# Optimization experiments

Measured on AMD Instinct MI355X. Metric: run time of the kernel, lower is better.

Reference implementation:

```python
import jax, jax.numpy as jnp
import numpy as np

K = 8
EPS = 1e-8


def setup_inputs() -> dict:
    key = jax.random.key(0)
    tokens = jax.random.normal(key, (32, 1024, 256), dtype=jnp.float32)
    return {"tokens": tokens}


def reference(tokens) -> jnp.ndarray:
    # tokens: [B, N, D] -> adjacency [B, N, N] float32 (0/1), mutual kNN, no self-loops
    B, N, D = tokens.shape
    tn = tokens / (jnp.linalg.norm(tokens, axis=-1, keepdims=True) + EPS)
    sim = jnp.einsum('bnd,bmd->bnm', tn, tn)  # [B, N, N] cosine similarity
    # mask diagonal (add_self=False)
    diag = jnp.eye(N, dtype=bool)
    sim = jnp.where(diag[None, :, :], -jnp.inf, sim)
    k = min(K, N - 1)
    _, topk_idx = jax.lax.top_k(sim, k)  # [B, N, k]
    b_idx = jnp.arange(B)[:, None, None]
    r_idx = jnp.arange(N)[None, :, None]
    adj = jnp.zeros((B, N, N), dtype=bool).at[b_idx, r_idx, topk_idx].set(True)
    # mutual kNN: keep edge only if both directions selected
    adj = adj & jnp.swapaxes(adj, 1, 2)
    return adj.astype(jnp.float32)
```

## Files before the change

kernel.cpp:

```cpp
#include <hip/hip_runtime.h>
#include <math.h>
#include <stdint.h>

#define B_ 32
#define N_ 1024
#define D_ 256
#define K_ 8
#define CAND 12

typedef unsigned short u16;
typedef unsigned int u32;
typedef __attribute__((ext_vector_type(8))) short s16x8;
typedef __attribute__((ext_vector_type(16))) float f32x16;

__device__ inline void cp16(const void* g, void* l) {
    __builtin_amdgcn_global_load_lds((const __attribute__((address_space(1))) void*)g,
                                     (__attribute__((address_space(3))) void*)l, 16, 0, 0);
}

__device__ inline u16 f2bf(float f) {
    uint32_t u = __float_as_uint(f);
    return (u16)((u + 0x7fffu + ((u >> 16) & 1u)) >> 16);
}
__device__ inline float bf2f(u16 h) { return __uint_as_float(((uint32_t)h) << 16); }
__device__ inline u32 umax32(u32 a, u32 b) { return a > b ? a : b; }
__device__ inline u32 umin32(u32 a, u32 b) { return a < b ? a : b; }

__global__ __launch_bounds__(256) void prep_kernel(const float* __restrict__ tok,
                                                   double* __restrict__ invn,
                                                   u16* __restrict__ xhi,
                                                   u16* __restrict__ xlo) {
    const int tid = threadIdx.x;
    const int wave = tid >> 6, lane = tid & 63;
    const int row = blockIdx.x * 4 + wave;
    const float4 v = *reinterpret_cast<const float4*>(tok + (size_t)row * D_ + lane * 4);
    double s = (double)v.x * v.x + (double)v.y * v.y +
               (double)v.z * v.z + (double)v.w * v.w;
    #pragma unroll
    for (int off = 32; off > 0; off >>= 1) s += __shfl_xor(s, off, 64);
    const double inv = 1.0 / (sqrt(s) + 1e-8);
    if (lane == 0) invn[row] = inv;
    const float x0 = (float)(v.x * inv), x1 = (float)(v.y * inv),
                x2 = (float)(v.z * inv), x3 = (float)(v.w * inv);
    ushort4 h, l;
    h.x = f2bf(x0); l.x = f2bf(x0 - bf2f(h.x));
    h.y = f2bf(x1); l.y = f2bf(x1 - bf2f(h.y));
    h.z = f2bf(x2); l.z = f2bf(x2 - bf2f(h.z));
    h.w = f2bf(x3); l.w = f2bf(x3 - bf2f(h.w));
    *reinterpret_cast<ushort4*>(xhi + (size_t)row * D_ + lane * 4) = h;
    *reinterpret_cast<ushort4*>(xlo + (size_t)row * D_ + lane * 4) = l;
}

__global__ __launch_bounds__(256, 3) void sim_topk_kernel(const u16* __restrict__ Xhi,
                                                          const u16* __restrict__ Xlo,
                                                          u32* __restrict__ candk,
                                                          int* __restrict__ candj) {
    __shared__ __align__(16) char smem[32768];
    char* tiles = smem;
    u32*  keysL = (u32*)smem;

    const int id    = blockIdx.x;
    const int chunk = id >> 3;
    const int b   = (id & 7) * 4 + (chunk >> 5);
    const int rem = chunk & 31;
    const int i0  = (rem >> 1) * 64;
    const int jh  = rem & 1;

    const int tid = threadIdx.x;
    const int w = tid >> 6, lane = tid & 63;
    const int mq = w >> 1, nq = w & 1;
    const int half = lane >> 5;
    const int il = lane & 31;

    const u16* XhiB = Xhi + (size_t)b * N_ * D_;
    const u16* XloB = Xlo + (size_t)b * N_ * D_;

    const int srr = lane >> 3, spp = lane & 7;
    const u16* ssrc = (w < 2) ? XhiB : XloB;
    const int  sgoff = (spp ^ srr) * 8;
    const int  srow  = (w & 1) * 32 + srr;
    char* const sbase = tiles + ((w < 2) ? 0 : 8192) + (w & 1) * 4096;

    const int ra = mq * 32 + il;
    const int rb = nq * 32 + il;
    const int xa = ra & 7, xb = rb & 7;

    s16x8 Ahf[4][4], Alf[4][4];
    #pragma unroll
    for (int kc = 0; kc < 4; ++kc) {
        __syncthreads();
        #pragma unroll
        for (int t = 0; t < 4; ++t) {
            const int rr = srow + t * 8;
            cp16(ssrc + (size_t)(i0 + rr) * D_ + kc * 64 + sgoff, sbase + t * 1024);
        }
        __syncthreads();
        #pragma unroll
        for (int ks = 0; ks < 4; ++ks) {
            const int ca = ((ks * 2 + half) ^ xa) * 16;
            Ahf[kc][ks] = *(const s16x8*)(tiles +        ra * 128 + ca);
            Alf[kc][ks] = *(const s16x8*)(tiles + 8192 + ra * 128 + ca);
        }
    }
    __syncthreads();

    auto STAGE_B = [&](int round, int bufn) {
        const int j0n = (jh * 8 + (round >> 2)) * 64;
        const int kcn = round & 3;
        char* bdst = sbase + bufn * 16384;
        #pragma unroll
        for (int t = 0; t < 4; ++t) {
            const int rr = srow + t * 8;
            cp16(ssrc + (size_t)(j0n + rr) * D_ + kcn * 64 + sgoff, bdst + t * 1024);
        }
    };

    const int diag_jt = i0 >> 6;
    u32 keys[CAND];
    #pragma unroll
    for (int c = 0; c < CAND; ++c) keys[c] = 0u;

    STAGE_B(0, 0);

    for (int lt = 0; lt < 8; ++lt) {
        const int jt = jh * 8 + lt;
        f32x16 acc;
        #pragma unroll
        for (int c = 0; c < 16; ++c) acc[c] = 0.0f;

        #pragma unroll
        for (int kc = 0; kc < 4; ++kc) {
            const int r = lt * 4 + kc;
            const int cur = r & 1;
            if (r < 31) {
                STAGE_B(r + 1, cur ^ 1);
                asm volatile("s_waitcnt vmcnt(4)" ::: "memory");
            } else {
                asm volatile("s_waitcnt vmcnt(0)" ::: "memory");
            }
            __builtin_amdgcn_s_barrier();
            __builtin_amdgcn_sched_barrier(0);
            const char* bb = tiles + cur * 16384;
            #pragma unroll
            for (int ks = 0; ks < 4; ++ks) {
                const int cb = ((ks * 2 + half) ^ xb) * 16;
                const s16x8 bh = *(const s16x8*)(bb +        rb * 128 + cb);
                const s16x8 bl = *(const s16x8*)(bb + 8192 + rb * 128 + cb);
                acc = __builtin_amdgcn_mfma_f32_32x32x16_bf16(bh, Ahf[kc][ks], acc, 0, 0, 0);
                acc = __builtin_amdgcn_mfma_f32_32x32x16_bf16(bl, Ahf[kc][ks], acc, 0, 0, 0);
                acc = __builtin_amdgcn_mfma_f32_32x32x16_bf16(bh, Alf[kc][ks], acc, 0, 0, 0);
            }
            __builtin_amdgcn_sched_barrier(0);
            __builtin_amdgcn_s_barrier();
        }

        const u32 codebase = (u32)(jt << 4);
        const bool diag = (jt == diag_jt) && (mq == nq);
        #pragma unroll
        for (int rg = 0; rg < 16; ++rg) {
            const u32 u = __float_as_uint(acc[rg]);
            const u32 mono = u ^ ((u32)(((int)u) >> 31) | 0x80000000u);
            u32 key = (mono & 0xFFFFFF00u) | (codebase + (u32)rg);
            if (diag && ((rg & 3) + 8 * (rg >> 2) + 4 * half == il)) key = 0u;
            u32 t = key;
            #pragma unroll
            for (int c = 0; c < CAND; ++c) {
                const u32 hi = umax32(keys[c], t);
                t = umin32(keys[c], t);
                keys[c] = hi;
            }
        }
    }

    __syncthreads();
    {
        const int r = mq * 32 + il;
        const int s = nq * 2 + half;
        u32* dst = keysL + (r * 4 + s) * CAND;
        #pragma unroll
        for (int c = 0; c < CAND; ++c) dst[c] = keys[c];
    }
    __syncthreads();

    if (tid < 64) {
        const u32* kl = keysL + tid * (4 * CAND);
        const size_t base = ((size_t)(b * N_ + i0 + tid) * 2 + jh) * CAND;
        int p0 = 0, p1 = 0, p2 = 0, p3 = 0;
        #pragma unroll
        for (int o = 0; o < CAND; ++o) {
            const u32 k0v = kl[p0];
            const u32 k1v = kl[CAND + p1];
            const u32 k2v = kl[2 * CAND + p2];
            const u32 k3v = kl[3 * CAND + p3];
            int bg = 0; u32 bv = k0v;
            if (k1v > bv) { bv = k1v; bg = 1; }
            if (k2v > bv) { bv = k2v; bg = 2; }
            if (k3v > bv) { bv = k3v; bg = 3; }
            const int code = (int)(bv & 0xFFu);
            const int jtv = code >> 4, rg = code & 15;
            candk[base + o] = bv;
            candj[base + o] = jtv * 64 + (bg >> 1) * 32 + (rg & 3) + 8 * (rg >> 2)
                              + 4 * (bg & 1);
            p0 += (bg == 0); p1 += (bg == 1); p2 += (bg == 2); p3 += (bg == 3);
        }
    }
}

__global__ __launch_bounds__(512) void merge_rescore_kernel(const u32* __restrict__ candk,
                                                            const int* __restrict__ candj,
                                                            const float* __restrict__ tok,
                                                            const double* __restrict__ invn,
                                                            int* __restrict__ topk) {
    __shared__ int    mj[64 * CAND];
    __shared__ double dv[64 * CAND];
    const int tid = threadIdx.x;

    const int id    = blockIdx.x;
    const int chunk = id >> 3;
    const int b     = (id & 7) * 4 + (chunk >> 4);
    const int i0    = (chunk & 15) * 64;
    const int R0    = b * N_ + i0;

    if (tid < 64) {
        const size_t base = (size_t)(R0 + tid) * 2 * CAND;
        int p0 = 0, p1 = 0;
        #pragma unroll
        for (int o = 0; o < CAND; ++o) {
            const u32 k0 = candk[base + p0];
            const u32 k1 = candk[base + CAND + p1];
            if (k0 >= k1) { mj[tid * CAND + o] = candj[base + p0];        ++p0; }
            else          { mj[tid * CAND + o] = candj[base + CAND + p1]; ++p1; }
        }
    }
    __syncthreads();

    {
        const int q = tid >> 2, ql = tid & 3;
        const int r = q >> 1;
        const float* qi = tok + (size_t)(R0 + r) * D_;
        const double di = invn[R0 + r];
        #pragma unroll 1
        for (int rr = 0; rr < 6; ++rr) {
            const int c = (q & 1) * 6 + rr;
            const int j = mj[r * CAND + c];
            const float* qj = tok + (size_t)(b * N_ + j) * D_;
            double s = 0.0;
            #pragma unroll 4
            for (int k = 0; k < 16; ++k) {
                const float4 x = *reinterpret_cast<const float4*>(qi + k * 16 + ql * 4);
                const float4 y = *reinterpret_cast<const float4*>(qj + k * 16 + ql * 4);
                s += (double)x.x * y.x + (double)x.y * y.y +
                     (double)x.z * y.z + (double)x.w * y.w;
            }
            s += __shfl_xor(s, 1, 64);
            s += __shfl_xor(s, 2, 64);
            if (ql == 0) dv[r * CAND + c] = s * di * invn[b * N_ + j];
        }
    }
    __syncthreads();

    if (tid < 64) {
        const int out_base = (R0 + tid) * K_;
        #pragma unroll 1
        for (int c = 0; c < CAND; ++c) {
            const double dc = dv[tid * CAND + c]; const int jc = mj[tid * CAND + c];
            int rank = 0;
            #pragma unroll 1
            for (int c2 = 0; c2 < CAND; ++c2) {
                if (c2 == c) continue;
                const double d2 = dv[tid * CAND + c2]; const int j2 = mj[tid * CAND + c2];
                if (d2 > dc || (d2 == dc && j2 < jc)) ++rank;
            }
            if (rank < K_) topk[out_base + rank] = jc;
        }
    }
}

__global__ __launch_bounds__(256) void mutual_kernel(const int* __restrict__ topk,
                                                     float* __restrict__ out) {
    const int gid = blockIdx.x * 256 + threadIdx.x;
    const int row = gid >> 3, s = gid & 7;
    const int j = topk[row * K_ + s];
    const int i = row & (N_ - 1);
    const int* tj = topk + ((row & ~(N_ - 1)) + j) * K_;
    bool m = false;
    #pragma unroll
    for (int u = 0; u < K_; ++u) m = m || (tj[u] == i);
    if (m) out[(size_t)row * N_ + j] = 1.0f;
}

extern "C" void kernel_launch(void* const* d_in, const int* in_sizes, int n_in,
                              void* d_out, int out_size, void* d_ws, size_t ws_size,
                              hipStream_t stream) {
    const float* tok = (const float*)d_in[0];
    float* out = (float*)d_out;
    double* invn = (double*)d_ws;
    int* topk = (int*)((char*)d_ws + (size_t)B_ * N_ * sizeof(double));
    u16* xhi = (u16*)d_out;
    u16* xlo = xhi + (size_t)B_ * N_ * D_;
    u32* candk = (u32*)((char*)d_out + (size_t)32 * 1024 * 1024);
    int* candj = (int*)((char*)d_out + (size_t)35 * 1024 * 1024);

    prep_kernel<<<dim3(B_ * N_ / 4), 256, 0, stream>>>(tok, invn, xhi, xlo);
    sim_topk_kernel<<<dim3(1024), 256, 0, stream>>>(xhi, xlo, candk, candj);
    merge_rescore_kernel<<<dim3(B_ * N_ / 64), 512, 0, stream>>>(candk, candj, tok, invn, topk);
    hipMemsetAsync(d_out, 0, (size_t)out_size * sizeof(float), stream);
    mutual_kernel<<<dim3(B_ * N_ * K_ / 256), 256, 0, stream>>>(topk, out);
}
```

Baseline: 301.3 us.

## Drop bf16 hi/lo split, use single bf16 similarity pass with rescore

Removes the low-order bf16 residual tensor and the two extra MFMAs per step, so the candidate similarity is computed with a single bf16 product instead of a three-term split. LDS tiles halve in size, occupancy hint rises to 4 blocks, and prep writes only one bf16 array. The merge/rescore kernel now handles 32 rows per block, with more threads per row and twice the block count. The risk is that lower-precision candidate scores may miss true top-k neighbours within the 12-candidate window before the exact fp64 rescore.

Result: faster. 258.9 us (-14.1%).

```diff
diff --git a/kernel.cpp b/kernel.cpp
--- a/kernel.cpp
+++ b/kernel.cpp
@@ -22,14 +22,12 @@
     uint32_t u = __float_as_uint(f);
     return (u16)((u + 0x7fffu + ((u >> 16) & 1u)) >> 16);
 }
-__device__ inline float bf2f(u16 h) { return __uint_as_float(((uint32_t)h) << 16); }
 __device__ inline u32 umax32(u32 a, u32 b) { return a > b ? a : b; }
 __device__ inline u32 umin32(u32 a, u32 b) { return a < b ? a : b; }
 
 __global__ __launch_bounds__(256) void prep_kernel(const float* __restrict__ tok,
                                                    double* __restrict__ invn,
-                                                   u16* __restrict__ xhi,
-                                                   u16* __restrict__ xlo) {
+                                                   u16* __restrict__ xhi) {
     const int tid = threadIdx.x;
     const int wave = tid >> 6, lane = tid & 63;
     const int row = blockIdx.x * 4 + wave;
@@ -40,22 +38,18 @@
     for (int off = 32; off > 0; off >>= 1) s += __shfl_xor(s, off, 64);
     const double inv = 1.0 / (sqrt(s) + 1e-8);
     if (lane == 0) invn[row] = inv;
-    const float x0 = (float)(v.x * inv), x1 = (float)(v.y * inv),
-                x2 = (float)(v.z * inv), x3 = (float)(v.w * inv);
-    ushort4 h, l;
-    h.x = f2bf(x0); l.x = f2bf(x0 - bf2f(h.x));
-    h.y = f2bf(x1); l.y = f2bf(x1 - bf2f(h.y));
-    h.z = f2bf(x2); l.z = f2bf(x2 - bf2f(h.z));
-    h.w = f2bf(x3); l.w = f2bf(x3 - bf2f(h.w));
+    ushort4 h;
+    h.x = f2bf((float)(v.x * inv));
+    h.y = f2bf((float)(v.y * inv));
+    h.z = f2bf((float)(v.z * inv));
+    h.w = f2bf((float)(v.w * inv));
     *reinterpret_cast<ushort4*>(xhi + (size_t)row * D_ + lane * 4) = h;
-    *reinterpret_cast<ushort4*>(xlo + (size_t)row * D_ + lane * 4) = l;
-}
-
-__global__ __launch_bounds__(256, 3) void sim_topk_kernel(const u16* __restrict__ Xhi,
-                                                          const u16* __restrict__ Xlo,
+}
+
+__global__ __launch_bounds__(256, 4) void sim_topk_kernel(const u16* __restrict__ Xhi,
                                                           u32* __restrict__ candk,
                                                           int* __restrict__ candj) {
-    __shared__ __align__(16) char smem[32768];
+    __shared__ __align__(16) char smem[16384];
     char* tiles = smem;
     u32*  keysL = (u32*)smem;
 
@@ -73,33 +67,30 @@
     const int il = lane & 31;
 
     const u16* XhiB = Xhi + (size_t)b * N_ * D_;
-    const u16* XloB = Xlo + (size_t)b * N_ * D_;
 
     const int srr = lane >> 3, spp = lane & 7;
-    const u16* ssrc = (w < 2) ? XhiB : XloB;
-    const int  sgoff = (spp ^ srr) * 8;
-    const int  srow  = (w & 1) * 32 + srr;
-    char* const sbase = tiles + ((w < 2) ? 0 : 8192) + (w & 1) * 4096;
+    const int sgoff = (spp ^ srr) * 8;
+    const int srow  = w * 16 + srr;
 
     const int ra = mq * 32 + il;
     const int rb = nq * 32 + il;
     const int xa = ra & 7, xb = rb & 7;
 
-    s16x8 Ahf[4][4], Alf[4][4];
+    s16x8 Ahf[4][4];
     #pragma unroll
     for (int kc = 0; kc < 4; ++kc) {
         __syncthreads();
         #pragma unroll
-        for (int t = 0; t < 4; ++t) {
+        for (int t = 0; t < 2; ++t) {
             const int rr = srow + t * 8;
-            cp16(ssrc + (size_t)(i0 + rr) * D_ + kc * 64 + sgoff, sbase + t * 1024);
+            cp16(XhiB + (size_t)(i0 + rr) * D_ + kc * 64 + sgoff,
+                 tiles + w * 2048 + t * 1024);
         }
         __syncthreads();
         #pragma unroll
         for (int ks = 0; ks < 4; ++ks) {
             const int ca = ((ks * 2 + half) ^ xa) * 16;
-            Ahf[kc][ks] = *(const s16x8*)(tiles +        ra * 128 + ca);
-            Alf[kc][ks] = *(const s16x8*)(tiles + 8192 + ra * 128 + ca);
+            Ahf[kc][ks] = *(const s16x8*)(tiles + ra * 128 + ca);
         }
     }
     __syncthreads();
@@ -107,11 +98,11 @@
     auto STAGE_B = [&](int round, int bufn) {
         const int j0n = (jh * 8 + (round >> 2)) * 64;
         const int kcn = round & 3;
-        char* bdst = sbase + bufn * 16384;
-        #pragma unroll
-        for (int t = 0; t < 4; ++t) {
+        char* bdst = tiles + bufn * 8192 + w * 2048;
+        #pragma unroll
+        for (int t = 0; t < 2; ++t) {
             const int rr = srow + t * 8;
-            cp16(ssrc + (size_t)(j0n + rr) * D_ + kcn * 64 + sgoff, bdst + t * 1024);
+            cp16(XhiB + (size_t)(j0n + rr) * D_ + kcn * 64 + sgoff, bdst + t * 1024);
         }
     };
 
@@ -134,21 +125,18 @@
             const int cur = r & 1;
             if (r < 31) {
                 STAGE_B(r + 1, cur ^ 1);
-                asm volatile("s_waitcnt vmcnt(4)" ::: "memory");
+                asm volatile("s_waitcnt vmcnt(2)" ::: "memory");
             } else {
                 asm volatile("s_waitcnt vmcnt(0)" ::: "memory");
             }
             __builtin_amdgcn_s_barrier();
             __builtin_amdgcn_sched_barrier(0);
-            const char* bb = tiles + cur * 16384;
+            const char* bb = tiles + cur * 8192;
             #pragma unroll
             for (int ks = 0; ks < 4; ++ks) {
                 const int cb = ((ks * 2 + half) ^ xb) * 16;
-                const s16x8 bh = *(const s16x8*)(bb +        rb * 128 + cb);
-                const s16x8 bl = *(const s16x8*)(bb + 8192 + rb * 128 + cb);
+                const s16x8 bh = *(const s16x8*)(bb + rb * 128 + cb);
                 acc = __builtin_amdgcn_mfma_f32_32x32x16_bf16(bh, Ahf[kc][ks], acc, 0, 0, 0);
-                acc = __builtin_amdgcn_mfma_f32_32x32x16_bf16(bl, Ahf[kc][ks], acc, 0, 0, 0);
-                acc = __builtin_amdgcn_mfma_f32_32x32x16_bf16(bh, Alf[kc][ks], acc, 0, 0, 0);
             }
             __builtin_amdgcn_sched_barrier(0);
             __builtin_amdgcn_s_barrier();
@@ -211,17 +199,17 @@
                                                             const float* __restrict__ tok,
                                                             const double* __restrict__ invn,
                                                             int* __restrict__ topk) {
-    __shared__ int    mj[64 * CAND];
-    __shared__ double dv[64 * CAND];
+    __shared__ int    mj[32 * CAND];
+    __shared__ double dv[32 * CAND];
     const int tid = threadIdx.x;
 
     const int id    = blockIdx.x;
     const int chunk = id >> 3;
-    const int b     = (id & 7) * 4 + (chunk >> 4);
-    const int i0    = (chunk & 15) * 64;
+    const int b     = (id & 7) * 4 + (chunk >> 5);
+    const int i0    = (chunk & 31) * 32;
     const int R0    = b * N_ + i0;
 
-    if (tid < 64) {
+    if (tid < 32) {
         const size_t base = (size_t)(R0 + tid) * 2 * CAND;
         int p0 = 0, p1 = 0;
         #pragma unroll
@@ -236,12 +224,12 @@
 
     {
         const int q = tid >> 2, ql = tid & 3;
-        const int r = q >> 1;
+        const int r = q >> 2;
         const float* qi = tok + (size_t)(R0 + r) * D_;
         const double di = invn[R0 + r];
         #pragma unroll 1
-        for (int rr = 0; rr < 6; ++rr) {
-            const int c = (q & 1) * 6 + rr;
+        for (int rr = 0; rr < 3; ++rr) {
+            const int c = (q & 3) * 3 + rr;
             const int j = mj[r * CAND + c];
             const float* qj = tok + (size_t)(b * N_ + j) * D_;
             double s = 0.0;
@@ -259,7 +247,7 @@
     }
     __syncthreads();
 
-    if (tid < 64) {
+    if (tid < 32) {
         const int out_base = (R0 + tid) * K_;
         #pragma unroll 1
         for (int c = 0; c < CAND; ++c) {
@@ -297,13 +285,12 @@
     double* invn = (double*)d_ws;
     int* topk = (int*)((char*)d_ws + (size_t)B_ * N_ * sizeof(double));
     u16* xhi = (u16*)d_out;
-    u16* xlo = xhi + (size_t)B_ * N_ * D_;
     u32* candk = (u32*)((char*)d_out + (size_t)32 * 1024 * 1024);
     int* candj = (int*)((char*)d_out + (size_t)35 * 1024 * 1024);
 
-    prep_kernel<<<dim3(B_ * N_ / 4), 256, 0, stream>>>(tok, invn, xhi, xlo);
-    sim_topk_kernel<<<dim3(1024), 256, 0, stream>>>(xhi, xlo, candk, candj);
-    merge_rescore_kernel<<<dim3(B_ * N_ / 64), 512, 0, stream>>>(candk, candj, tok, invn, topk);
+    prep_kernel<<<dim3(B_ * N_ / 4), 256, 0, stream>>>(tok, invn, xhi);
+    sim_topk_kernel<<<dim3(1024), 256, 0, stream>>>(xhi, candk, candj);
+    merge_rescore_kernel<<<dim3(B_ * N_ / 32), 512, 0, stream>>>(candk, candj, tok, invn, topk);
     hipMemsetAsync(d_out, 0, (size_t)out_size * sizeof(float), stream);
     mutual_kernel<<<dim3(B_ * N_ * K_ / 256), 256, 0, stream>>>(topk, out);
 }
```
